# Kernel tuning notes

Measured on AMD Instinct MI355X. Metric: run time of the kernel, lower is better.

The kernel has to match this reference:

```python
import jax, jax.numpy as jnp
import numpy as np

TOPK, NUM_CLASSES = 13, 80
ALPHA, BETA, GAMMA, EPS = 1.0, 5.0, 3.0, 1e-09


def _make_boxes(key, shape, img=640.0, wmin=10.0, wmax=120.0):
    k1, k2 = jax.random.split(key)
    cxy = jax.random.uniform(k1, shape[:-1] + (2,), minval=0.0, maxval=img)
    wh = jax.random.uniform(k2, shape[:-1] + (2,), minval=wmin, maxval=wmax)
    return jnp.concatenate([cxy - wh / 2, cxy + wh / 2], axis=-1)


def setup_inputs() -> dict:
    key = jax.random.key(0)
    ks = jax.random.split(key, 7)
    bs, A, C, n = 16, 8400, 80, 60
    return {
        'pd_scores': jax.random.uniform(ks[0], (bs, A, C), dtype=jnp.float32),
        'pd_bboxes': _make_boxes(ks[1], (bs, A, 4)),
        'pd_angles': jax.random.uniform(ks[2], (bs, A, 1), minval=0.0, maxval=90.0),
        'anc_points': jax.random.uniform(ks[3], (A, 2), minval=0.0, maxval=640.0),
        'gt_labels': jax.random.randint(ks[4], (bs, n, 1), 0, C, dtype=jnp.int32),
        'gt_bboxes': _make_boxes(ks[5], (bs, n, 4)),
        'gt_angles': jax.random.uniform(ks[6], (bs, n, 1), minval=0.0, maxval=90.0),
        'mask_gt': jnp.ones((bs, n, 1), jnp.float32),
        'epoch_num': 1,
    }


def _cos_fn(x, ar, beta=2.0):
    return 0.5 + 0.5 * jnp.cos(beta / ar * x / 180.0 * jnp.pi + jnp.pi * (1.0 - beta / (2.0 * ar)))


def _angle_measure(pd_angles, gt_angles, gt_bboxes):
    # gt area ratio w/h -> (bs, n, 1, 1)
    w = gt_bboxes[..., 2:3] - gt_bboxes[..., 0:1]
    h = gt_bboxes[..., 3:4] - gt_bboxes[..., 1:2]
    ar = (w / (h + 1e-05))[:, :, None, :]
    theta = jnp.abs(gt_angles[:, :, None, :] - pd_angles[:, None, :, :])  # (bs,n,A,1)
    av = 1.0 / ar / (2.0 - 1.0 / ar)
    mx = _cos_fn(0.0, ar)
    mn = _cos_fn(90.0, ar)
    r = (_cos_fn(theta, ar) - mn) / (mx - mn) * (1.0 - av) + av
    r = jnp.where(jnp.isnan(r), 0.0, r)
    return jnp.squeeze(r, -1)  # (bs, n, A)


def _pairwise_iou(gt, pd):
    # gt (bs,n,4), pd (bs,A,4) -> (bs,n,A)
    lt = jnp.maximum(gt[:, :, None, :2], pd[:, None, :, :2])
    rb = jnp.minimum(gt[:, :, None, 2:], pd[:, None, :, 2:])
    inter = jnp.clip(rb - lt, 0.0).prod(-1)
    a1 = jnp.clip(gt[..., 2:] - gt[..., :2], 0.0).prod(-1)[:, :, None]
    a2 = jnp.clip(pd[..., 2:] - pd[..., :2], 0.0).prod(-1)[:, None, :]
    return inter / (a1 + a2 - inter + EPS)


def _select_topk(metrics, topk_mask):
    bs, n, A = metrics.shape
    _, idxs = jax.lax.top_k(metrics, TOPK)
    idxs = jnp.where(topk_mask, idxs, 0)
    flat = idxs.reshape(bs * n, TOPK)
    cnt = jnp.zeros((bs * n, A), jnp.int32).at[jnp.arange(bs * n)[:, None], flat].add(1)
    cnt = cnt.reshape(bs, n, A)
    return jnp.where(cnt > 1, 0, cnt).astype(metrics.dtype)


def _select_highest_overlaps(mask_pos, overlaps, n):
    fg = mask_pos.sum(-2)                                   # (bs, A)
    multi = fg[:, None, :] > 1                              # (bs, 1, A)
    is_max = jax.nn.one_hot(overlaps.argmax(1), n, axis=1, dtype=mask_pos.dtype)  # (bs,n,A)
    mask_pos = jnp.where(multi, is_max, mask_pos)
    fg = mask_pos.sum(-2)
    tgt_idx = mask_pos.argmax(-2)                           # (bs, A)
    return tgt_idx, fg, mask_pos


def reference(pd_scores, pd_bboxes, pd_angles, anc_points, gt_labels, gt_bboxes, gt_angles, mask_gt, epoch_num):
    bs, A, C = pd_scores.shape
    n = gt_bboxes.shape[1]
    lab = gt_labels[..., 0].astype(jnp.int32)               # (bs, n)

    # bbox_scores: pd_scores[b, :, gt_label] -> (bs, n, A)
    pts = jnp.transpose(pd_scores, (0, 2, 1))               # (bs, C, A)
    bbox_scores = jnp.take_along_axis(pts, lab[:, :, None], axis=1)

    overlaps = _pairwise_iou(gt_bboxes, pd_bboxes)          # (bs, n, A)
    ang = _angle_measure(pd_angles, gt_angles, gt_bboxes)   # (bs, n, A)
    align = bbox_scores ** ALPHA * overlaps ** BETA * ang ** GAMMA

    # anchors-inside-gt mask (bs, n, A)
    lt = anc_points[None, None, :, :] - gt_bboxes[:, :, None, :2]
    rb = gt_bboxes[:, :, None, 2:] - anc_points[None, None, :, :]
    in_gts = (jnp.concatenate([lt, rb], -1).min(-1) > EPS).astype(align.dtype)

    topk_mask = jnp.broadcast_to(mask_gt > 0, (bs, n, TOPK))
    mask_topk = _select_topk(align * in_gts, topk_mask)
    mask_pos = mask_topk * in_gts * mask_gt                 # (bs, n, A)

    tgt_idx, fg, mask_pos = _select_highest_overlaps(mask_pos, overlaps, n)

    # gather per-anchor targets from flattened gt tensors
    off = tgt_idx + jnp.arange(bs, dtype=tgt_idx.dtype)[:, None] * n   # (bs, A)
    tlab = lab.reshape(-1)[off]
    tlab = jnp.where(tlab < 0, 0, tlab)
    tbb = gt_bboxes.reshape(-1, 4)[off]                     # (bs, A, 4)
    tang = gt_angles.reshape(-1, 1)[off]                    # (bs, A, 1)
    ts = jax.nn.one_hot(tlab, C, dtype=pd_scores.dtype)     # (bs, A, C)
    ts = jnp.where(fg[:, :, None] > 0, ts, 0.0)

    # normalized alignment metric scaling
    align = align * mask_pos
    pam = align.max(-1, keepdims=True)                      # (bs, n, 1)
    pov = (overlaps * mask_pos).max(-1, keepdims=True)      # (bs, n, 1)
    norm = (align * pov / (pam + EPS)).max(-2)[:, :, None]  # (bs, A, 1)
    ts = ts * norm

    return tlab, tbb, tang, ts, fg > 0
```

## Files before the change

### kernel.cpp

```cpp
#include <hip/hip_runtime.h>
#include <math.h>

#define TOPK 13
#define PI_F 3.14159265358979323846f
#define K1_THREADS 512
#define K1_WAVES (K1_THREADS / 64)

typedef unsigned int u32;
typedef unsigned long long u64;

__device__ __forceinline__ u32 ford(float f) {
    u32 u = __float_as_uint(f);
    return (u & 0x80000000u) ? ~u : (u | 0x80000000u);
}
__device__ __forceinline__ float funord(u32 o) {
    u32 u = (o & 0x80000000u) ? (o & 0x7FFFFFFFu) : ~o;
    return __uint_as_float(u);
}

__device__ __forceinline__ float iou_fn(float4 g, float4 p) {
    float ltx = fmaxf(g.x, p.x), lty = fmaxf(g.y, p.y);
    float rbx = fminf(g.z, p.z), rby = fminf(g.w, p.w);
    float inter = fmaxf(rbx - ltx, 0.0f) * fmaxf(rby - lty, 0.0f);
    float a1 = fmaxf(g.z - g.x, 0.0f) * fmaxf(g.w - g.y, 0.0f);
    float a2 = fmaxf(p.z - p.x, 0.0f) * fmaxf(p.w - p.y, 0.0f);
    return inter / (((a1 + a2) - inter) + 1e-9f);
}

struct RowParams { float av, bar, offc, mx, mn; };

__device__ __forceinline__ RowParams row_params(float4 g) {
    float w = g.z - g.x, h = g.w - g.y;
    float ar = w / (h + 1e-5f);
    float ia = 1.0f / ar;
    RowParams rp;
    rp.av = ia / (2.0f - ia);
    rp.bar = 2.0f / ar;
    rp.offc = PI_F * (1.0f - 2.0f / (2.0f * ar));
    rp.mx = 0.5f + 0.5f * cosf(rp.offc);
    rp.mn = 0.5f + 0.5f * cosf(rp.bar * 90.0f / 180.0f * PI_F + rp.offc);
    return rp;
}

__device__ __forceinline__ float ang_measure(const RowParams& rp, float theta) {
    float cfv = 0.5f + 0.5f * cosf(rp.bar * theta / 180.0f * PI_F + rp.offc);
    float r = (cfv - rp.mn) / (rp.mx - rp.mn) * (1.0f - rp.av) + rp.av;
    return isnan(r) ? 0.0f : r;
}

__device__ __forceinline__ float align_fn(float s, float iou, float r) {
    float iou2 = iou * iou;
    float iou5 = (iou2 * iou2) * iou;
    float r3 = (r * r) * r;
    return (s * iou5) * r3;
}

__device__ __forceinline__ void ins13(u64* arr, u64 key) {
#pragma unroll
    for (int jj = 0; jj < TOPK; jj++) {
        u64 hi = arr[jj] > key ? arr[jj] : key;
        u64 lo = arr[jj] > key ? key : arr[jj];
        arr[jj] = hi;
        key = lo;
    }
}

__global__ void k0_init(int* cnt, int* assign1, u32* pam, u32* pov, int BA, int BN) {
    int t = blockIdx.x * blockDim.x + threadIdx.x;
    if (t < BA) { cnt[t] = 0; assign1[t] = -1; }
    if (t < BN) { pam[t] = 0x80000000u; pov[t] = 0x80000000u; }
}

__global__ __launch_bounds__(K1_THREADS)
void k1_topk(const float* __restrict__ scores, const float* __restrict__ pbox,
             const float* __restrict__ pang, const float* __restrict__ anc,
             const int* __restrict__ glab, const float* __restrict__ gbox,
             const float* __restrict__ gang, const float* __restrict__ mgt,
             int* __restrict__ cnt, int* __restrict__ assign1,
             int bs, int A, int n, int C) {
    int j = blockIdx.x;
    int b = j % bs;
    int i = j / bs;
    int bi = b * n + i;
    int tid = threadIdx.x;
    int lane = tid & 63, wv = tid >> 6;

    float mg = mgt[bi];
    if (!(mg > 0.0f)) return;

    float4 g = ((const float4*)gbox)[bi];
    int lab = glab[bi];
    float ga = gang[bi];
    RowParams rp = row_params(g);

    const float4* pb = ((const float4*)pbox) + (size_t)b * A;
    const float* pa = pang + (size_t)b * A;
    const float2* ac = (const float2*)anc;
    const float* sc = scores + (size_t)b * A * C + lab;

    u64 arr[TOPK];
#pragma unroll
    for (int jj = 0; jj < TOPK; jj++) arr[jj] = 0ull;
    u64 zkey = 0ull;

    bool zc0 = false;
    {
        int a = tid;
        float4 p = pb[a];
        float iou = iou_fn(g, p);
        float2 apt = ac[a];
        float mnv = fminf(fminf(apt.x - g.x, apt.y - g.y), fminf(g.z - apt.x, g.w - apt.y));
        bool hot = (mnv > 1e-9f) && iou > 0.0f;
        float th = fabsf(ga - pa[a]);
        float r = ang_measure(rp, th);
        if (hot && r > 0.0f) {
            float s = sc[(size_t)a * C];
            float v = align_fn(s, iou, r);
            if (v > 0.0f) {
                u64 key = ((u64)ford(v) << 32) | (u64)(0xFFFFFFFFu - (u32)a);
                ins13(arr, key);
            } else {
                zc0 = true;
            }
        } else {
            zc0 = (r >= 0.0f);
        }
        if (zc0) zkey = (0x80000000ull << 32) | (u64)(0xFFFFFFFFu - (u32)a);
    }
    __shared__ int s_zc[K1_WAVES];
    u64 bal = __ballot(zc0);
    if (lane == 0) s_zc[wv] = __popcll(bal);
    __syncthreads();
    int zc = 0;
#pragma unroll
    for (int w = 0; w < K1_WAVES; w++) zc += s_zc[w];

    if (zc >= TOPK) {
        for (int a = tid + K1_THREADS; a < A; a += K1_THREADS) {
            float4 p = pb[a];
            float iou = iou_fn(g, p);
            float2 apt = ac[a];
            float mnv = fminf(fminf(apt.x - g.x, apt.y - g.y), fminf(g.z - apt.x, g.w - apt.y));
            bool hot = (mnv > 1e-9f) && iou > 0.0f;
            if (hot) {
                float th = fabsf(ga - pa[a]);
                float r = ang_measure(rp, th);
                if (r > 0.0f) {
                    float s = sc[(size_t)a * C];
                    float v = align_fn(s, iou, r);
                    if (v > 0.0f) {
                        u64 key = ((u64)ford(v) << 32) | (u64)(0xFFFFFFFFu - (u32)a);
                        if (key > arr[TOPK - 1]) ins13(arr, key);
                    }
                }
            }
        }
    } else {
        for (int a = tid + K1_THREADS; a < A; a += K1_THREADS) {
            float4 p = pb[a];
            float iou = iou_fn(g, p);
            float2 apt = ac[a];
            float mnv = fminf(fminf(apt.x - g.x, apt.y - g.y), fminf(g.z - apt.x, g.w - apt.y));
            bool hot = (mnv > 1e-9f) && iou > 0.0f;
            float th = fabsf(ga - pa[a]);
            float r = ang_measure(rp, th);
            bool zeroCand;
            if (hot && r > 0.0f) {
                float s = sc[(size_t)a * C];
                float v = align_fn(s, iou, r);
                if (v > 0.0f) {
                    zeroCand = false;
                    u64 key = ((u64)ford(v) << 32) | (u64)(0xFFFFFFFFu - (u32)a);
                    if (key > arr[TOPK - 1]) ins13(arr, key);
                } else {
                    zeroCand = true;
                }
            } else {
                zeroCand = (r >= 0.0f);
            }
            if (zeroCand && zkey == 0ull) {
                zkey = (0x80000000ull << 32) | (u64)(0xFFFFFFFFu - (u32)a);
            }
        }
    }
    if (zkey > arr[TOPK - 1]) ins13(arr, zkey);

    __shared__ u64 sh[2][K1_WAVES];
    for (int round = 0; round < TOPK; round++) {
        u64 head = arr[0];
        u64 m = head;
#pragma unroll
        for (int st = 32; st > 0; st >>= 1) {
            u64 o = __shfl_xor(m, st, 64);
            if (o > m) m = o;
        }
        if (lane == 0) sh[round & 1][wv] = m;
        __syncthreads();
        u64 win = sh[round & 1][0];
#pragma unroll
        for (int w = 1; w < K1_WAVES; w++) {
            u64 o = sh[round & 1][w]; if (o > win) win = o;
        }
        if (head == win && win != 0ull) {
#pragma unroll
            for (int jj = 0; jj < TOPK - 1; jj++) arr[jj] = arr[jj + 1];
            arr[TOPK - 1] = 0ull;
            int a = (int)(0xFFFFFFFFu - (u32)(win & 0xFFFFFFFFull));
            float2 apt = ac[a];
            float mnv = fminf(fminf(apt.x - g.x, apt.y - g.y), fminf(g.z - apt.x, g.w - apt.y));
            if (mnv > 1e-9f) {
                atomicAdd(&cnt[(size_t)b * A + a], 1);
                atomicMax(&assign1[(size_t)b * A + a], i);
            }
        }
    }
}

__global__ __launch_bounds__(256)
void k2_resolve(const float* __restrict__ scores, const float* __restrict__ pbox,
                const float* __restrict__ pang, const int* __restrict__ glab,
                const float* __restrict__ gbox, const float* __restrict__ gang,
                const int* __restrict__ cnt, const int* __restrict__ assign1,
                int* __restrict__ assign, float* __restrict__ alignv,
                u32* __restrict__ pam, u32* __restrict__ pov,
                int bs, int A, int n, int C) {
    int t = blockIdx.x * blockDim.x + threadIdx.x;
    if (t >= bs * A) return;
    int b = t / A;
    int c = cnt[t];
    int asg = -1;
    float alv = 0.0f;
    if (c > 0) {
        float4 p = ((const float4*)pbox)[t];
        if (c == 1) {
            asg = assign1[t];
        } else {
            float best = -1.0f;
            asg = 0;
            for (int i = 0; i < n; i++) {
                float4 gi = ((const float4*)gbox)[b * n + i];
                float io = iou_fn(gi, p);
                if (io > best) { best = io; asg = i; }
            }
        }
        float4 g = ((const float4*)gbox)[b * n + asg];
        RowParams rp = row_params(g);
        float iou = iou_fn(g, p);
        float th = fabsf(gang[b * n + asg] - pang[t]);
        float r = ang_measure(rp, th);
        float s = scores[(size_t)t * C + glab[b * n + asg]];
        alv = align_fn(s, iou, r);
        atomicMax(&pam[b * n + asg], ford(alv));
        atomicMax(&pov[b * n + asg], ford(iou));
    }
    assign[t] = asg;
    alignv[t] = alv;
}

__global__ __launch_bounds__(256)
void k3_out(const int* __restrict__ glab, const float* __restrict__ gbox,
            const float* __restrict__ gang, const int* __restrict__ assign,
            const float* __restrict__ alignv, const u32* __restrict__ pam,
            const u32* __restrict__ pov, float* __restrict__ out,
            int bs, int A, int n, int C) {
    __shared__ float s_nv[256];
    __shared__ int s_lf[256];
    int tid = threadIdx.x;
    int base = blockIdx.x * 256;
    int t = base + tid;
    int BA = bs * A;

    if (t < BA) {
        int b = t / A;
        int asg = assign[t];
        bool fg = asg >= 0;
        int tgt = fg ? asg : 0;
        int lb = glab[b * n + tgt];
        if (lb < 0) lb = 0;

        float* o_tlab = out;
        float* o_tbb = out + BA;
        float* o_tang = out + (size_t)BA * 5;
        float* o_fg = out + (size_t)BA * 6 + (size_t)BA * C;

        o_tlab[t] = (float)lb;
        ((float4*)o_tbb)[t] = ((const float4*)gbox)[b * n + tgt];
        o_tang[t] = gang[b * n + tgt];
        o_fg[t] = fg ? 1.0f : 0.0f;

        float nv = 0.0f;
        if (fg) {
            float pamv = funord(pam[b * n + asg]);
            float povv = funord(pov[b * n + asg]);
            float vv = (alignv[t] * povv) / (pamv + 1e-9f);
            nv = fmaxf(vv, 0.0f);
        }
        s_nv[tid] = nv;
        s_lf[tid] = fg ? lb : -1;
    } else {
        s_nv[tid] = 0.0f;
        s_lf[tid] = -1;
    }
    __syncthreads();

    int Q = C / 4;
    int nA = min(256, BA - base);
    if (nA <= 0) return;
    int total = nA * Q;
    float4* o_ts = (float4*)(out + (size_t)BA * 6) + (size_t)base * Q;
    for (int idx = tid; idx < total; idx += 256) {
        int tl = idx / Q;
        int q = idx - tl * Q;
        float nv = s_nv[tl];
        int lf = s_lf[tl];
        int cb = q * 4;
        float4 o;
        o.x = (lf == cb) ? nv : 0.0f;
        o.y = (lf == cb + 1) ? nv : 0.0f;
        o.z = (lf == cb + 2) ? nv : 0.0f;
        o.w = (lf == cb + 3) ? nv : 0.0f;
        o_ts[idx] = o;
    }
}

extern "C" void kernel_launch(void* const* d_in, const int* in_sizes, int n_in,
                              void* d_out, int out_size, void* d_ws, size_t ws_size,
                              hipStream_t stream) {
    const float* scores = (const float*)d_in[0];
    const float* pbox = (const float*)d_in[1];
    const float* pang = (const float*)d_in[2];
    const float* anc = (const float*)d_in[3];
    const int* glab = (const int*)d_in[4];
    const float* gbox = (const float*)d_in[5];
    const float* gang = (const float*)d_in[6];
    const float* mgt = (const float*)d_in[7];

    const int C = 80;
    int A = in_sizes[3] / 2;
    int bs = in_sizes[0] / (A * C);
    int n = in_sizes[4] / bs;
    int BA = bs * A;
    int BN = bs * n;

    char* ws = (char*)d_ws;
    int* cnt = (int*)ws;        ws += sizeof(int) * (size_t)BA;
    int* assign1 = (int*)ws;    ws += sizeof(int) * (size_t)BA;
    int* assign = (int*)ws;     ws += sizeof(int) * (size_t)BA;
    float* alignv = (float*)ws; ws += sizeof(float) * (size_t)BA;
    u32* pam = (u32*)ws;        ws += sizeof(u32) * (size_t)BN;
    u32* pov = (u32*)ws;        ws += sizeof(u32) * (size_t)BN;

    k0_init<<<(BA + 255) / 256, 256, 0, stream>>>(cnt, assign1, pam, pov, BA, BN);
    k1_topk<<<BN, K1_THREADS, 0, stream>>>(scores, pbox, pang, anc, glab, gbox, gang, mgt,
                                           cnt, assign1, bs, A, n, C);
    k2_resolve<<<(BA + 255) / 256, 256, 0, stream>>>(scores, pbox, pang, glab, gbox, gang,
                                                     cnt, assign1, assign, alignv, pam, pov,
                                                     bs, A, n, C);
    k3_out<<<(BA + 255) / 256, 256, 0, stream>>>(glab, gbox, gang, assign, alignv, pam, pov,
                                                 (float*)d_out, bs, A, n, C);
}
```

Baseline: 185.7 us.

## Bin anchors into spatial grid to scan only cells overlapping each gt box

Adds a single-block kernel that buckets anchor points into a 10x10 grid of 64-pixel cells. In the common top-k path, each gt row then visits only the anchors in cells its box overlaps, instead of scanning all 8400 anchors. Block size also drops from 512 to 256, which changes which anchors the first-pass zero-candidate check covers. The extra launch is serial, with one block doing shared-memory atomics, and the scan order changes.

```diff
diff --git a/kernel.cpp b/kernel.cpp
--- a/kernel.cpp
+++ b/kernel.cpp
@@ -3,8 +3,10 @@
 
 #define TOPK 13
 #define PI_F 3.14159265358979323846f
-#define K1_THREADS 512
+#define K1_THREADS 256
 #define K1_WAVES (K1_THREADS / 64)
+#define GC 10
+#define INV_CELL (1.0f / 64.0f)
 
 typedef unsigned int u32;
 typedef unsigned long long u64;
@@ -71,11 +73,49 @@
     if (t < BN) { pam[t] = 0x80000000u; pov[t] = 0x80000000u; }
 }
 
+__global__ __launch_bounds__(1024)
+void k_grid(const float* __restrict__ anc, int A,
+            int* __restrict__ cell_start, float2* __restrict__ cell_pts,
+            u32* __restrict__ cell_idx) {
+    __shared__ int s_cnt[GC * GC];
+    __shared__ int s_off[GC * GC + 1];
+    int tid = threadIdx.x;
+    if (tid < GC * GC) s_cnt[tid] = 0;
+    __syncthreads();
+    const float2* ac = (const float2*)anc;
+    for (int a = tid; a < A; a += 1024) {
+        float2 p = ac[a];
+        int cx = min(GC - 1, max(0, (int)(p.x * INV_CELL)));
+        int cy = min(GC - 1, max(0, (int)(p.y * INV_CELL)));
+        atomicAdd(&s_cnt[cy * GC + cx], 1);
+    }
+    __syncthreads();
+    if (tid == 0) {
+        int acc = 0;
+        for (int c = 0; c < GC * GC; c++) { s_off[c] = acc; acc += s_cnt[c]; }
+        s_off[GC * GC] = acc;
+    }
+    __syncthreads();
+    if (tid <= GC * GC) cell_start[tid] = s_off[tid];
+    if (tid < GC * GC) s_cnt[tid] = s_off[tid];
+    __syncthreads();
+    for (int a = tid; a < A; a += 1024) {
+        float2 p = ac[a];
+        int cx = min(GC - 1, max(0, (int)(p.x * INV_CELL)));
+        int cy = min(GC - 1, max(0, (int)(p.y * INV_CELL)));
+        int pos = atomicAdd(&s_cnt[cy * GC + cx], 1);
+        cell_pts[pos] = p;
+        cell_idx[pos] = (u32)a;
+    }
+}
+
 __global__ __launch_bounds__(K1_THREADS)
 void k1_topk(const float* __restrict__ scores, const float* __restrict__ pbox,
              const float* __restrict__ pang, const float* __restrict__ anc,
              const int* __restrict__ glab, const float* __restrict__ gbox,
              const float* __restrict__ gang, const float* __restrict__ mgt,
+             const int* __restrict__ cell_start, const float2* __restrict__ cell_pts,
+             const u32* __restrict__ cell_idx,
              int* __restrict__ cnt, int* __restrict__ assign1,
              int bs, int A, int n, int C) {
     int j = blockIdx.x;
@@ -102,6 +142,8 @@
 #pragma unroll
     for (int jj = 0; jj < TOPK; jj++) arr[jj] = 0ull;
     u64 zkey = 0ull;
+
+    __shared__ int s_zc[K1_WAVES];
 
     bool zc0 = false;
     {
@@ -127,30 +169,41 @@
         }
         if (zc0) zkey = (0x80000000ull << 32) | (u64)(0xFFFFFFFFu - (u32)a);
     }
-    __shared__ int s_zc[K1_WAVES];
-    u64 bal = __ballot(zc0);
-    if (lane == 0) s_zc[wv] = __popcll(bal);
+    u64 bal0 = __ballot(zc0);
+    if (lane == 0) s_zc[wv] = __popcll(bal0);
     __syncthreads();
     int zc = 0;
 #pragma unroll
     for (int w = 0; w < K1_WAVES; w++) zc += s_zc[w];
 
     if (zc >= TOPK) {
-        for (int a = tid + K1_THREADS; a < A; a += K1_THREADS) {
-            float4 p = pb[a];
-            float iou = iou_fn(g, p);
-            float2 apt = ac[a];
-            float mnv = fminf(fminf(apt.x - g.x, apt.y - g.y), fminf(g.z - apt.x, g.w - apt.y));
-            bool hot = (mnv > 1e-9f) && iou > 0.0f;
-            if (hot) {
-                float th = fabsf(ga - pa[a]);
-                float r = ang_measure(rp, th);
-                if (r > 0.0f) {
-                    float s = sc[(size_t)a * C];
-                    float v = align_fn(s, iou, r);
-                    if (v > 0.0f) {
-                        u64 key = ((u64)ford(v) << 32) | (u64)(0xFFFFFFFFu - (u32)a);
-                        if (key > arr[TOPK - 1]) ins13(arr, key);
+        int cx0 = max(0, (int)floorf(g.x * INV_CELL));
+        int cx1 = min(GC - 1, (int)floorf(g.z * INV_CELL));
+        int cy0 = max(0, (int)floorf(g.y * INV_CELL));
+        int cy1 = min(GC - 1, (int)floorf(g.w * INV_CELL));
+        for (int cy = cy0; cy <= cy1; cy++) {
+            for (int cx = cx0; cx <= cx1; cx++) {
+                int cs = cell_start[cy * GC + cx];
+                int ce = cell_start[cy * GC + cx + 1];
+                for (int t2 = cs + tid; t2 < ce; t2 += K1_THREADS) {
+                    u32 a = cell_idx[t2];
+                    if (a < K1_THREADS) continue;
+                    float2 apt = cell_pts[t2];
+                    float mnv = fminf(fminf(apt.x - g.x, apt.y - g.y),
+                                      fminf(g.z - apt.x, g.w - apt.y));
+                    if (!(mnv > 1e-9f)) continue;
+                    float4 p = pb[a];
+                    float iou = iou_fn(g, p);
+                    if (!(iou > 0.0f)) continue;
+                    float th = fabsf(ga - pa[a]);
+                    float r = ang_measure(rp, th);
+                    if (r > 0.0f) {
+                        float s = sc[(size_t)a * C];
+                        float v = align_fn(s, iou, r);
+                        if (v > 0.0f) {
+                            u64 key = ((u64)ford(v) << 32) | (u64)(0xFFFFFFFFu - a);
+                            if (key > arr[TOPK - 1]) ins13(arr, key);
+                        }
                     }
                 }
             }
@@ -343,15 +396,21 @@
     int BN = bs * n;
 
     char* ws = (char*)d_ws;
-    int* cnt = (int*)ws;        ws += sizeof(int) * (size_t)BA;
-    int* assign1 = (int*)ws;    ws += sizeof(int) * (size_t)BA;
-    int* assign = (int*)ws;     ws += sizeof(int) * (size_t)BA;
-    float* alignv = (float*)ws; ws += sizeof(float) * (size_t)BA;
-    u32* pam = (u32*)ws;        ws += sizeof(u32) * (size_t)BN;
-    u32* pov = (u32*)ws;        ws += sizeof(u32) * (size_t)BN;
+    int* cnt = (int*)ws;          ws += sizeof(int) * (size_t)BA;
+    int* assign1 = (int*)ws;      ws += sizeof(int) * (size_t)BA;
+    int* assign = (int*)ws;       ws += sizeof(int) * (size_t)BA;
+    float* alignv = (float*)ws;   ws += sizeof(float) * (size_t)BA;
+    u32* pam = (u32*)ws;          ws += sizeof(u32) * (size_t)BN;
+    u32* pov = (u32*)ws;          ws += sizeof(u32) * (size_t)BN;
+    int* cell_start = (int*)ws;   ws += sizeof(int) * (GC * GC + 1);
+    ws = (char*)(((size_t)ws + 7) & ~(size_t)7);
+    float2* cell_pts = (float2*)ws; ws += sizeof(float2) * (size_t)A;
+    u32* cell_idx = (u32*)ws;     ws += sizeof(u32) * (size_t)A;
 
     k0_init<<<(BA + 255) / 256, 256, 0, stream>>>(cnt, assign1, pam, pov, BA, BN);
+    k_grid<<<1, 1024, 0, stream>>>(anc, A, cell_start, cell_pts, cell_idx);
     k1_topk<<<BN, K1_THREADS, 0, stream>>>(scores, pbox, pang, anc, glab, gbox, gang, mgt,
+                                           cell_start, cell_pts, cell_idx,
                                            cnt, assign1, bs, A, n, C);
     k2_resolve<<<(BA + 255) / 256, 256, 0, stream>>>(scores, pbox, pang, glab, gbox, gang,
                                                      cnt, assign1, assign, alignv, pam, pov,
```

After: 174.7 us. 5.9% less time.
